# Optimization experiments

Measured on AMD Instinct MI355X. Metric: run time of the kernel, lower is better.

## Reference

```python
import jax, jax.numpy as jnp
import numpy as np

T, B, I, H = 512, 64, 512, 512

def setup_inputs() -> dict:
    key = jax.random.key(0)
    ks = jax.random.split(key, 9)
    s = 1.0 / np.sqrt(I + H)
    return {
        "inputs": jax.random.normal(ks[0], (T, B, I), dtype=jnp.float32),
        "Wf": jax.random.normal(ks[1], (H, I + H), dtype=jnp.float32) * s,
        "bf": jax.random.normal(ks[2], (H,), dtype=jnp.float32) * s,
        "Wi": jax.random.normal(ks[3], (H, I + H), dtype=jnp.float32) * s,
        "bi": jax.random.normal(ks[4], (H,), dtype=jnp.float32) * s,
        "Wg": jax.random.normal(ks[5], (H, I + H), dtype=jnp.float32) * s,
        "bg": jax.random.normal(ks[6], (H,), dtype=jnp.float32) * s,
        "Wo": jax.random.normal(ks[7], (H, I + H), dtype=jnp.float32) * s,
        "bo": jax.random.normal(ks[8], (H,), dtype=jnp.float32) * s,
    }

def reference(inputs, Wf, bf, Wi, bi, Wg, bg, Wo, bo):
    # Stack the 4 gate linears into one GEMM per step: W_all [4H, I+H]
    W_all = jnp.concatenate([Wf, Wi, Wg, Wo], axis=0)
    b_all = jnp.concatenate([bf, bi, bg, bo], axis=0)
    h = inputs.shape[1], Wf.shape[0]
    hx0 = jnp.zeros((inputs.shape[1], Wf.shape[0]), dtype=inputs.dtype)
    cx0 = jnp.zeros_like(hx0)

    def step(carry, x):
        hx, cx = carry
        combined = jnp.concatenate([x, hx], axis=1)        # [B, I+H]
        gates = combined @ W_all.T + b_all                 # [B, 4H]
        f_raw, i_raw, g_raw, o_raw = jnp.split(gates, 4, axis=1)
        f = jax.nn.sigmoid(f_raw)
        i = jax.nn.sigmoid(i_raw)
        g = jnp.tanh(g_raw)
        o = jax.nn.sigmoid(o_raw)
        cx = f * cx + i * g
        hx = o * jnp.tanh(cx)
        return (hx, cx), hx

    (hx, cx), stacked = jax.lax.scan(step, (hx0, cx0), inputs)
    return stacked, hx, cx
```

## Files before the change

kernel.cpp:

```cpp
#include <hip/hip_runtime.h>
#include <hip/hip_bf16.h>
#include <stdint.h>

typedef __bf16 bf16_t;
typedef __bf16 bf16x8 __attribute__((ext_vector_type(8)));
typedef __bf16 bf16x4_t __attribute__((ext_vector_type(4)));
typedef float f32x4 __attribute__((ext_vector_type(4)));
typedef uint32_t u32x4 __attribute__((ext_vector_type(4)));

#define T_STEPS 512
#define B_SZ 64
#define I_SZ 512
#define H_SZ 512
#define NB 4
#define BS 16
#define NC 32
#define CS 16

#define XBF_OFF   0ull
#define WBF_OFF   33554432ull
#define BALL_OFF  (WBF_OFF + 4194304ull)
#define HEXP_OFF  (BALL_OFF + 8192ull)

__device__ __forceinline__ float sigmoid_fast(float x) {
  return 1.f / (1.f + __expf(-x));
}
__device__ __forceinline__ float tanh_fast(float x) {
  float xc = fminf(fmaxf(x, -10.f), 10.f);
  float e = __expf(2.f * xc);
  return (e - 1.f) / (e + 1.f);
}

__device__ __forceinline__ u32x4 load_b128_cc(const void* addr) {
  u32x4 v;
  asm volatile("global_load_dwordx4 %0, %1, off sc0 sc1"
               : "=v"(v) : "v"(addr) : "memory");
  return v;
}
__device__ __forceinline__ void store_b32_cc(void* addr, uint32_t v) {
  asm volatile("global_store_dword %0, %1, off sc0 sc1"
               :: "v"(addr), "v"(v) : "memory");
}
__device__ __forceinline__ void wait_vm0() {
  asm volatile("s_waitcnt vmcnt(0)" ::: "memory");
}

__global__ void prep_x(const float* __restrict__ x, bf16_t* __restrict__ xbf) {
  const int nch = (T_STEPS * B_SZ * I_SZ) / 8;
  int c = blockIdx.x * blockDim.x + threadIdx.x;
  int stride = gridDim.x * blockDim.x;
  for (; c < nch; c += stride) {
    int lane = c & 63;
    int kt = (c >> 6) & 7;
    int w  = (c >> 9) & 1;
    int bg = (c >> 10) & 3;
    int t  = c >> 12;
    int r = lane & 15, quad = lane >> 4;
    const float* src = x + ((size_t)t * B_SZ + bg * BS + r) * I_SZ + w * 256 + kt * 32 + quad * 8;
    float4 lo = *(const float4*)src;
    float4 hi = *(const float4*)(src + 4);
    bf16x8 o = { (bf16_t)lo.x, (bf16_t)lo.y, (bf16_t)lo.z, (bf16_t)lo.w,
                 (bf16_t)hi.x, (bf16_t)hi.y, (bf16_t)hi.z, (bf16_t)hi.w };
    *(bf16x8*)(xbf + (size_t)c * 8) = o;
  }
}

__global__ void prep_rest(const float* __restrict__ wf, const float* __restrict__ wi,
                          const float* __restrict__ wgm, const float* __restrict__ wo,
                          const float* __restrict__ bfv, const float* __restrict__ biv,
                          const float* __restrict__ bgv, const float* __restrict__ bov,
                          bf16_t* __restrict__ wbf, float* __restrict__ ball,
                          uint32_t* __restrict__ hexp) {
  int gtid = blockIdx.x * blockDim.x + threadIdx.x;
  int stride = gridDim.x * blockDim.x;
  const int WCH = (2048 * 1024) / 4;
  for (int i = gtid; i < WCH; i += stride) {
    int r = i >> 8;
    int c = (i & 255) << 2;
    int g = r >> 9, sr = r & 511;
    const float* src = (g == 0) ? wf : (g == 1) ? wi : (g == 2) ? wgm : wo;
    float4 v = *(const float4*)(src + (size_t)sr * 1024 + c);
    bf16x4_t o = { (bf16_t)v.x, (bf16_t)v.y, (bf16_t)v.z, (bf16_t)v.w };
    *(bf16x4_t*)(wbf + (size_t)r * 1024 + c) = o;
  }
  for (int i = gtid; i < 2048; i += stride) {
    int g = i >> 9;
    const float* src = (g == 0) ? bfv : (g == 1) ? biv : (g == 2) ? bgv : bov;
    ball[i] = src[i & 511];
  }
  for (int i = gtid; i < 65536; i += stride) hexp[i] = 0;
}

__global__ __launch_bounds__(256, 1) void qlstm_main(
    const bf16_t* __restrict__ xbf, const bf16_t* __restrict__ wbf,
    const float* __restrict__ ball, uint32_t* __restrict__ hexp,
    float* __restrict__ out) {
  const int wg = blockIdx.x;
  const int bg = wg >> 5;
  const int ic = wg & 31;
  const int tid = threadIdx.x;
  const int wave = tid >> 6;
  const int lane = tid & 63;
  const int l15 = lane & 15;
  const int quad = lane >> 4;
  const int kq = wave * 4;

  __shared__ __align__(16) float Gp[2][4][16][68];

  bf16x8 wfr[4][8];
#pragma unroll
  for (int g = 0; g < 4; ++g) {
    const bf16_t* wp = wbf + ((size_t)(g * 512 + ic * CS + l15)) * 1024 + quad * 8;
#pragma unroll
    for (int j = 0; j < 4; ++j) {
      wfr[g][j]     = *(const bf16x8*)(wp + (kq + j) * 32);
      wfr[g][4 + j] = *(const bf16x8*)(wp + 512 + (kq + j) * 32);
    }
  }

  int off[4];
#pragma unroll
  for (int j = 0; j < 4; ++j)
    off[j] = (((kq + j) >> 3) << 12) + (((kq + j) & 7) << 9) + lane * 8;

  const int erow = tid >> 4;
  const int ecol = tid & 15;
  const float bias_f = ball[0 * 512 + ic * CS + ecol];
  const float bias_i = ball[1 * 512 + ic * CS + ecol];
  const float bias_g = ball[2 * 512 + ic * CS + ecol];
  const float bias_o = ball[3 * 512 + ic * CS + ecol];

  const int brow = bg * BS + erow;
  const int hcol = ic * CS + ecol;

  const int wh = hcol >> 8;
  const int kp = hcol & 255;
  const int pof = wh * 4096 + ((kp >> 5) << 9) + ((((kp >> 3) & 3) * 16 + erow) << 3) + (kp & 7);

  float c_state = 0.f, h = 0.f;
  const size_t out_hx = (size_t)T_STEPS * B_SZ * H_SZ;

  const bf16_t* xwb = xbf + ((size_t)bg << 13);

#pragma unroll 1
  for (int t = 0; t < T_STEPS; ++t) {
    const int par = t & 1;
    const uint32_t pat = (uint32_t)t << 16;

    f32x4 x0 = {0, 0, 0, 0}, x1 = {0, 0, 0, 0}, x2 = {0, 0, 0, 0}, x3 = {0, 0, 0, 0};
    {
      const bf16_t* xp = xwb + ((size_t)t << 15);
      bf16x8 fx0 = *(const bf16x8*)(xp + off[0]);
      bf16x8 fx1 = *(const bf16x8*)(xp + off[1]);
      bf16x8 fx2 = *(const bf16x8*)(xp + off[2]);
      bf16x8 fx3 = *(const bf16x8*)(xp + off[3]);
      x0 = __builtin_amdgcn_mfma_f32_16x16x32_bf16(fx0, wfr[0][0], x0, 0, 0, 0);
      x1 = __builtin_amdgcn_mfma_f32_16x16x32_bf16(fx0, wfr[1][0], x1, 0, 0, 0);
      x2 = __builtin_amdgcn_mfma_f32_16x16x32_bf16(fx0, wfr[2][0], x2, 0, 0, 0);
      x3 = __builtin_amdgcn_mfma_f32_16x16x32_bf16(fx0, wfr[3][0], x3, 0, 0, 0);
      x0 = __builtin_amdgcn_mfma_f32_16x16x32_bf16(fx1, wfr[0][1], x0, 0, 0, 0);
      x1 = __builtin_amdgcn_mfma_f32_16x16x32_bf16(fx1, wfr[1][1], x1, 0, 0, 0);
      x2 = __builtin_amdgcn_mfma_f32_16x16x32_bf16(fx1, wfr[2][1], x2, 0, 0, 0);
      x3 = __builtin_amdgcn_mfma_f32_16x16x32_bf16(fx1, wfr[3][1], x3, 0, 0, 0);
      x0 = __builtin_amdgcn_mfma_f32_16x16x32_bf16(fx2, wfr[0][2], x0, 0, 0, 0);
      x1 = __builtin_amdgcn_mfma_f32_16x16x32_bf16(fx2, wfr[1][2], x1, 0, 0, 0);
      x2 = __builtin_amdgcn_mfma_f32_16x16x32_bf16(fx2, wfr[2][2], x2, 0, 0, 0);
      x3 = __builtin_amdgcn_mfma_f32_16x16x32_bf16(fx2, wfr[3][2], x3, 0, 0, 0);
      x0 = __builtin_amdgcn_mfma_f32_16x16x32_bf16(fx3, wfr[0][3], x0, 0, 0, 0);
      x1 = __builtin_amdgcn_mfma_f32_16x16x32_bf16(fx3, wfr[1][3], x1, 0, 0, 0);
      x2 = __builtin_amdgcn_mfma_f32_16x16x32_bf16(fx3, wfr[2][3], x2, 0, 0, 0);
      x3 = __builtin_amdgcn_mfma_f32_16x16x32_bf16(fx3, wfr[3][3], x3, 0, 0, 0);
    }

    const uint32_t* hb = hexp + ((size_t)(((par ^ 1) * 4 + bg)) << 13);
    u32x4 v[8];
    for (;;) {
#pragma unroll
      for (int j = 0; j < 4; ++j) {
        v[2 * j]     = load_b128_cc(hb + off[j]);
        v[2 * j + 1] = load_b128_cc(hb + off[j] + 4);
      }
      wait_vm0();
      uint32_t bad = 0;
#pragma unroll
      for (int q = 0; q < 8; ++q)
        bad |= (v[q].x ^ pat) | (v[q].y ^ pat) | (v[q].z ^ pat) | (v[q].w ^ pat);
      if (__all((int)((bad & 0xffff0000u) == 0))) break;
      __builtin_amdgcn_s_sleep(1);
    }

    f32x4 a0 = x0, a1 = x1, a2 = x2, a3 = x3;
#pragma unroll
    for (int j = 0; j < 4; ++j) {
      u32x4 a = v[2 * j], b = v[2 * j + 1];
      union { uint32_t u[4]; bf16x8 fv2; } cv;
      cv.u[0] = (a.x & 0xffffu) | (a.y << 16);
      cv.u[1] = (a.z & 0xffffu) | (a.w << 16);
      cv.u[2] = (b.x & 0xffffu) | (b.y << 16);
      cv.u[3] = (b.z & 0xffffu) | (b.w << 16);
      a0 = __builtin_amdgcn_mfma_f32_16x16x32_bf16(cv.fv2, wfr[0][4 + j], a0, 0, 0, 0);
      a1 = __builtin_amdgcn_mfma_f32_16x16x32_bf16(cv.fv2, wfr[1][4 + j], a1, 0, 0, 0);
      a2 = __builtin_amdgcn_mfma_f32_16x16x32_bf16(cv.fv2, wfr[2][4 + j], a2, 0, 0, 0);
      a3 = __builtin_amdgcn_mfma_f32_16x16x32_bf16(cv.fv2, wfr[3][4 + j], a3, 0, 0, 0);
    }

#pragma unroll
    for (int i = 0; i < 4; ++i) {
      f32x4 pv = { a0[i], a1[i], a2[i], a3[i] };
      *(f32x4*)&Gp[par][wave][quad * 4 + i][l15 * 4] = pv;
    }
    __syncthreads();

    f32x4 s = *(const f32x4*)&Gp[par][0][erow][ecol * 4];
    s += *(const f32x4*)&Gp[par][1][erow][ecol * 4];
    s += *(const f32x4*)&Gp[par][2][erow][ecol * 4];
    s += *(const f32x4*)&Gp[par][3][erow][ecol * 4];

    float fg = sigmoid_fast(s[0] + bias_f);
    float ig = sigmoid_fast(s[1] + bias_i);
    float gg = tanh_fast(s[2] + bias_g);
    float og = sigmoid_fast(s[3] + bias_o);
    c_state = fg * c_state + ig * gg;
    h = og * tanh_fast(c_state);

    union { bf16_t b; unsigned short u; } cvt;
    cvt.b = (bf16_t)h;
    uint32_t pk = ((uint32_t)(t + 1) << 16) | (uint32_t)cvt.u;
    store_b32_cc(hexp + ((size_t)((par * 4 + bg)) << 13) + pof, pk);

    out[((size_t)t * B_SZ + brow) * H_SZ + hcol] = h;
  }

  out[out_hx + (size_t)brow * H_SZ + hcol] = h;
  out[out_hx + (size_t)(B_SZ * H_SZ) + (size_t)brow * H_SZ + hcol] = c_state;
}

extern "C" void kernel_launch(void* const* d_in, const int* in_sizes, int n_in,
                              void* d_out, int out_size, void* d_ws, size_t ws_size,
                              hipStream_t stream) {
  const float* x   = (const float*)d_in[0];
  const float* Wf  = (const float*)d_in[1];
  const float* bfv = (const float*)d_in[2];
  const float* Wi  = (const float*)d_in[3];
  const float* biv = (const float*)d_in[4];
  const float* Wg  = (const float*)d_in[5];
  const float* bgv = (const float*)d_in[6];
  const float* Wo  = (const float*)d_in[7];
  const float* bov = (const float*)d_in[8];
  float* out = (float*)d_out;

  char* ws = (char*)d_ws;
  bf16_t* xbf    = (bf16_t*)(ws + XBF_OFF);
  bf16_t* wbf    = (bf16_t*)(ws + WBF_OFF);
  float*  ball   = (float*)(ws + BALL_OFF);
  uint32_t* hexp = (uint32_t*)(ws + HEXP_OFF);

  prep_x<<<dim3(2048), dim3(256), 0, stream>>>(x, xbf);
  prep_rest<<<dim3(1024), dim3(256), 0, stream>>>(Wf, Wi, Wg, Wo, bfv, biv, bgv, bov,
                                                  wbf, ball, hexp);
  qlstm_main<<<dim3(NB * NC), dim3(256), 0, stream>>>(xbf, wbf, ball, hexp, out);
}
```

Before: 1.175 ms.

## Speculatively prefetch hidden-state tiles before x-projection MFMAs to hide poll latency

Each step now issues the x-tile loads and a first speculative coherent load of the previous step's hidden state before the input-projection MFMAs. A second coherent poll is issued after those MFMAs. If the first speculative read already carries the current step tag, it is consumed directly; otherwise the code falls back to polling with the second read. This aims to overlap global-load latency and cross-block synchronization with the x-side matrix work, at the cost of extra coherent traffic and higher register pressure.

After: 1.261 ms. +7.4%, slower.

```diff
diff --git a/kernel.cpp b/kernel.cpp
--- a/kernel.cpp
+++ b/kernel.cpp
@@ -31,6 +31,12 @@
   return (e - 1.f) / (e + 1.f);
 }
 
+__device__ __forceinline__ u32x4 load_b128(const void* addr) {
+  u32x4 v;
+  asm volatile("global_load_dwordx4 %0, %1, off"
+               : "=v"(v) : "v"(addr) : "memory");
+  return v;
+}
 __device__ __forceinline__ u32x4 load_b128_cc(const void* addr) {
   u32x4 v;
   asm volatile("global_load_dwordx4 %0, %1, off sc0 sc1"
@@ -43,6 +49,9 @@
 }
 __device__ __forceinline__ void wait_vm0() {
   asm volatile("s_waitcnt vmcnt(0)" ::: "memory");
+}
+__device__ __forceinline__ void wait_vm8() {
+  asm volatile("s_waitcnt vmcnt(8)" ::: "memory");
 }
 
 __global__ void prep_x(const float* __restrict__ x, bf16_t* __restrict__ xbf) {
@@ -146,62 +155,103 @@
   for (int t = 0; t < T_STEPS; ++t) {
     const int par = t & 1;
     const uint32_t pat = (uint32_t)t << 16;
+    const uint32_t* hb = hexp + ((size_t)(((par ^ 1) * 4 + bg)) << 13);
+
+    u32x4 xr0 = load_b128(xwb + ((size_t)t << 15) + off[0]);
+    u32x4 xr1 = load_b128(xwb + ((size_t)t << 15) + off[1]);
+    u32x4 xr2 = load_b128(xwb + ((size_t)t << 15) + off[2]);
+    u32x4 xr3 = load_b128(xwb + ((size_t)t << 15) + off[3]);
+    u32x4 vA[8];
+#pragma unroll
+    for (int j = 0; j < 4; ++j) {
+      vA[2 * j]     = load_b128_cc(hb + off[j]);
+      vA[2 * j + 1] = load_b128_cc(hb + off[j] + 4);
+    }
+    wait_vm8();
+    __builtin_amdgcn_sched_barrier(0);
 
     f32x4 x0 = {0, 0, 0, 0}, x1 = {0, 0, 0, 0}, x2 = {0, 0, 0, 0}, x3 = {0, 0, 0, 0};
     {
-      const bf16_t* xp = xwb + ((size_t)t << 15);
-      bf16x8 fx0 = *(const bf16x8*)(xp + off[0]);
-      bf16x8 fx1 = *(const bf16x8*)(xp + off[1]);
-      bf16x8 fx2 = *(const bf16x8*)(xp + off[2]);
-      bf16x8 fx3 = *(const bf16x8*)(xp + off[3]);
-      x0 = __builtin_amdgcn_mfma_f32_16x16x32_bf16(fx0, wfr[0][0], x0, 0, 0, 0);
-      x1 = __builtin_amdgcn_mfma_f32_16x16x32_bf16(fx0, wfr[1][0], x1, 0, 0, 0);
-      x2 = __builtin_amdgcn_mfma_f32_16x16x32_bf16(fx0, wfr[2][0], x2, 0, 0, 0);
-      x3 = __builtin_amdgcn_mfma_f32_16x16x32_bf16(fx0, wfr[3][0], x3, 0, 0, 0);
-      x0 = __builtin_amdgcn_mfma_f32_16x16x32_bf16(fx1, wfr[0][1], x0, 0, 0, 0);
-      x1 = __builtin_amdgcn_mfma_f32_16x16x32_bf16(fx1, wfr[1][1], x1, 0, 0, 0);
-      x2 = __builtin_amdgcn_mfma_f32_16x16x32_bf16(fx1, wfr[2][1], x2, 0, 0, 0);
-      x3 = __builtin_amdgcn_mfma_f32_16x16x32_bf16(fx1, wfr[3][1], x3, 0, 0, 0);
-      x0 = __builtin_amdgcn_mfma_f32_16x16x32_bf16(fx2, wfr[0][2], x0, 0, 0, 0);
-      x1 = __builtin_amdgcn_mfma_f32_16x16x32_bf16(fx2, wfr[1][2], x1, 0, 0, 0);
-      x2 = __builtin_amdgcn_mfma_f32_16x16x32_bf16(fx2, wfr[2][2], x2, 0, 0, 0);
-      x3 = __builtin_amdgcn_mfma_f32_16x16x32_bf16(fx2, wfr[3][2], x3, 0, 0, 0);
-      x0 = __builtin_amdgcn_mfma_f32_16x16x32_bf16(fx3, wfr[0][3], x0, 0, 0, 0);
-      x1 = __builtin_amdgcn_mfma_f32_16x16x32_bf16(fx3, wfr[1][3], x1, 0, 0, 0);
-      x2 = __builtin_amdgcn_mfma_f32_16x16x32_bf16(fx3, wfr[2][3], x2, 0, 0, 0);
-      x3 = __builtin_amdgcn_mfma_f32_16x16x32_bf16(fx3, wfr[3][3], x3, 0, 0, 0);
-    }
-
-    const uint32_t* hb = hexp + ((size_t)(((par ^ 1) * 4 + bg)) << 13);
-    u32x4 v[8];
-    for (;;) {
+      union { u32x4 u; bf16x8 f; } c0, c1, c2, c3;
+      c0.u = xr0; c1.u = xr1; c2.u = xr2; c3.u = xr3;
+      x0 = __builtin_amdgcn_mfma_f32_16x16x32_bf16(c0.f, wfr[0][0], x0, 0, 0, 0);
+      x1 = __builtin_amdgcn_mfma_f32_16x16x32_bf16(c0.f, wfr[1][0], x1, 0, 0, 0);
+      x2 = __builtin_amdgcn_mfma_f32_16x16x32_bf16(c0.f, wfr[2][0], x2, 0, 0, 0);
+      x3 = __builtin_amdgcn_mfma_f32_16x16x32_bf16(c0.f, wfr[3][0], x3, 0, 0, 0);
+      x0 = __builtin_amdgcn_mfma_f32_16x16x32_bf16(c1.f, wfr[0][1], x0, 0, 0, 0);
+      x1 = __builtin_amdgcn_mfma_f32_16x16x32_bf16(c1.f, wfr[1][1], x1, 0, 0, 0);
+      x2 = __builtin_amdgcn_mfma_f32_16x16x32_bf16(c1.f, wfr[2][1], x2, 0, 0, 0);
+      x3 = __builtin_amdgcn_mfma_f32_16x16x32_bf16(c1.f, wfr[3][1], x3, 0, 0, 0);
+      x0 = __builtin_amdgcn_mfma_f32_16x16x32_bf16(c2.f, wfr[0][2], x0, 0, 0, 0);
+      x1 = __builtin_amdgcn_mfma_f32_16x16x32_bf16(c2.f, wfr[1][2], x1, 0, 0, 0);
+      x2 = __builtin_amdgcn_mfma_f32_16x16x32_bf16(c2.f, wfr[2][2], x2, 0, 0, 0);
+      x3 = __builtin_amdgcn_mfma_f32_16x16x32_bf16(c2.f, wfr[3][2], x3, 0, 0, 0);
+      x0 = __builtin_amdgcn_mfma_f32_16x16x32_bf16(c3.f, wfr[0][3], x0, 0, 0, 0);
+      x1 = __builtin_amdgcn_mfma_f32_16x16x32_bf16(c3.f, wfr[1][3], x1, 0, 0, 0);
+      x2 = __builtin_amdgcn_mfma_f32_16x16x32_bf16(c3.f, wfr[2][3], x2, 0, 0, 0);
+      x3 = __builtin_amdgcn_mfma_f32_16x16x32_bf16(c3.f, wfr[3][3], x3, 0, 0, 0);
+    }
+    __builtin_amdgcn_sched_barrier(0);
+
+    u32x4 vB[8];
+#pragma unroll
+    for (int j = 0; j < 4; ++j) {
+      vB[2 * j]     = load_b128_cc(hb + off[j]);
+      vB[2 * j + 1] = load_b128_cc(hb + off[j] + 4);
+    }
+    wait_vm8();
+    __builtin_amdgcn_sched_barrier(0);
+
+    f32x4 a0 = x0, a1 = x1, a2 = x2, a3 = x3;
+    uint32_t badA = 0;
+#pragma unroll
+    for (int q = 0; q < 8; ++q)
+      badA |= (vA[q].x ^ pat) | (vA[q].y ^ pat) | (vA[q].z ^ pat) | (vA[q].w ^ pat);
+
+    if (__all((int)((badA & 0xffff0000u) == 0))) {
 #pragma unroll
       for (int j = 0; j < 4; ++j) {
-        v[2 * j]     = load_b128_cc(hb + off[j]);
-        v[2 * j + 1] = load_b128_cc(hb + off[j] + 4);
+        u32x4 a = vA[2 * j], b = vA[2 * j + 1];
+        union { uint32_t u[4]; bf16x8 fv2; } cv;
+        cv.u[0] = (a.x & 0xffffu) | (a.y << 16);
+        cv.u[1] = (a.z & 0xffffu) | (a.w << 16);
+        cv.u[2] = (b.x & 0xffffu) | (b.y << 16);
+        cv.u[3] = (b.z & 0xffffu) | (b.w << 16);
+        a0 = __builtin_amdgcn_mfma_f32_16x16x32_bf16(cv.fv2, wfr[0][4 + j], a0, 0, 0, 0);
+        a1 = __builtin_amdgcn_mfma_f32_16x16x32_bf16(cv.fv2, wfr[1][4 + j], a1, 0, 0, 0);
+        a2 = __builtin_amdgcn_mfma_f32_16x16x32_bf16(cv.fv2, wfr[2][4 + j], a2, 0, 0, 0);
+        a3 = __builtin_amdgcn_mfma_f32_16x16x32_bf16(cv.fv2, wfr[3][4 + j], a3, 0, 0, 0);
       }
+    } else {
       wait_vm0();
-      uint32_t bad = 0;
-#pragma unroll
-      for (int q = 0; q < 8; ++q)
-        bad |= (v[q].x ^ pat) | (v[q].y ^ pat) | (v[q].z ^ pat) | (v[q].w ^ pat);
-      if (__all((int)((bad & 0xffff0000u) == 0))) break;
-      __builtin_amdgcn_s_sleep(1);
-    }
-
-    f32x4 a0 = x0, a1 = x1, a2 = x2, a3 = x3;
-#pragma unroll
-    for (int j = 0; j < 4; ++j) {
-      u32x4 a = v[2 * j], b = v[2 * j + 1];
-      union { uint32_t u[4]; bf16x8 fv2; } cv;
-      cv.u[0] = (a.x & 0xffffu) | (a.y << 16);
-      cv.u[1] = (a.z & 0xffffu) | (a.w << 16);
-      cv.u[2] = (b.x & 0xffffu) | (b.y << 16);
-      cv.u[3] = (b.z & 0xffffu) | (b.w << 16);
-      a0 = __builtin_amdgcn_mfma_f32_16x16x32_bf16(cv.fv2, wfr[0][4 + j], a0, 0, 0, 0);
-      a1 = __builtin_amdgcn_mfma_f32_16x16x32_bf16(cv.fv2, wfr[1][4 + j], a1, 0, 0, 0);
-      a2 = __builtin_amdgcn_mfma_f32_16x16x32_bf16(cv.fv2, wfr[2][4 + j], a2, 0, 0, 0);
-      a3 = __builtin_amdgcn_mfma_f32_16x16x32_bf16(cv.fv2, wfr[3][4 + j], a3, 0, 0, 0);
+      __builtin_amdgcn_sched_barrier(0);
+      for (;;) {
+        uint32_t bad = 0;
+#pragma unroll
+        for (int q = 0; q < 8; ++q)
+          bad |= (vB[q].x ^ pat) | (vB[q].y ^ pat) | (vB[q].z ^ pat) | (vB[q].w ^ pat);
+        if (__all((int)((bad & 0xffff0000u) == 0))) break;
+#pragma unroll
+        for (int j = 0; j < 4; ++j) {
+          vB[2 * j]     = load_b128_cc(hb + off[j]);
+          vB[2 * j + 1] = load_b128_cc(hb + off[j] + 4);
+        }
+        wait_vm0();
+        __builtin_amdgcn_sched_barrier(0);
+      }
+#pragma unroll
+      for (int j = 0; j < 4; ++j) {
+        u32x4 a = vB[2 * j], b = vB[2 * j + 1];
+        union { uint32_t u[4]; bf16x8 fv2; } cv;
+        cv.u[0] = (a.x & 0xffffu) | (a.y << 16);
+        cv.u[1] = (a.z & 0xffffu) | (a.w << 16);
+        cv.u[2] = (b.x & 0xffffu) | (b.y << 16);
+        cv.u[3] = (b.z & 0xffffu) | (b.w << 16);
+        a0 = __builtin_amdgcn_mfma_f32_16x16x32_bf16(cv.fv2, wfr[0][4 + j], a0, 0, 0, 0);
+        a1 = __builtin_amdgcn_mfma_f32_16x16x32_bf16(cv.fv2, wfr[1][4 + j], a1, 0, 0, 0);
+        a2 = __builtin_amdgcn_mfma_f32_16x16x32_bf16(cv.fv2, wfr[2][4 + j], a2, 0, 0, 0);
+        a3 = __builtin_amdgcn_mfma_f32_16x16x32_bf16(cv.fv2, wfr[3][4 + j], a3, 0, 0, 0);
+      }
     }
 
 #pragma unroll
```
